# Performance work log

Measured on AMD Instinct MI355X. Metric: run time of the kernel, lower is better.

## Reference

```python
import jax, jax.numpy as jnp
import numpy as np
from jax import lax

B, L, C_IN, H = 2048, 128, 150, 230  # batch, seq_len, 3*word_size, hidden_size

MASK_TABLE = jnp.array([[0., 0., 0.],
                        [1., 0., 0.],
                        [0., 1., 0.],
                        [0., 0., 1.]], dtype=jnp.float32)  # frozen mask embedding


def setup_inputs() -> dict:
    key = jax.random.key(0)
    k1, k2, k3 = jax.random.split(key, 3)
    Xea = jax.random.normal(k1, (B, L, C_IN), dtype=jnp.float32)
    X_mask = jax.random.randint(k2, (B, L), 0, 4)
    # xavier_uniform for Conv1d weight [out, in, kw]
    fan_in, fan_out = C_IN * 3, H * 3
    limit = float(np.sqrt(6.0 / (fan_in + fan_out)))
    W = jax.random.uniform(k3, (H, C_IN, 3), dtype=jnp.float32, minval=-limit, maxval=limit)
    b = jnp.zeros((H,), dtype=jnp.float32)
    return {"Xea": Xea, "X_mask": X_mask, "W": W, "b": b}


def reference(Xea, X_mask, W, b):
    # Xea: [B, L, C_in] -> conv over sequence dim, kernel=3, padding=1
    x = jnp.transpose(Xea, (0, 2, 1))  # [B, C_in, L]
    y = lax.conv_general_dilated(
        x, W, window_strides=(1,), padding=[(1, 1)],
        dimension_numbers=('NCH', 'OIH', 'NCH'))  # [B, H, L]
    y = y + b[None, :, None]
    X = jnp.transpose(y, (0, 2, 1))  # [B, L, H]
    m = MASK_TABLE[X_mask]  # [B, L, 3] one-hot piece indicators (0 row = pad)
    # piecewise max pool: broadcast multiply then max over seq
    pooled = jnp.max(m[:, :, None, :] * X[:, :, :, None], axis=1)  # [B, H, 3]
    return jnp.tanh(pooled.reshape(pooled.shape[0], -1))  # [B, 3*H]
```

## Files before the change

kernel.cpp:

```cpp
#include <hip/hip_runtime.h>
#include <hip/hip_bf16.h>
#include <math.h>


#define B_SZ   2048
#define L_SEQ  128
#define C_INCH 150
#define H_OUT  230
#define RS     152
#define NROW   129
#define NS8    2451

typedef __attribute__((ext_vector_type(8))) short short8;
typedef __attribute__((ext_vector_type(4))) float float4v;

static __device__ __forceinline__ unsigned short f2bf(float f) {
    union { float f; unsigned u; } x{f};
    unsigned r = (x.u + 0x7FFFu + ((x.u >> 16) & 1u)) >> 16;
    return (unsigned short)r;
}

static __device__ __forceinline__ unsigned cvt2(float2 f) {
    __hip_bfloat162 h = __float22bfloat162_rn(f);
    union { __hip_bfloat162 h; unsigned u; } c{h};
    return c.u;
}

static __device__ __forceinline__ float tanh_fast_pos(float v) {
    float e = __expf(2.0f * v);
    return 1.0f - 2.0f / (e + 1.0f);
}

__global__ void pack_w_kernel(const float* __restrict__ W,
                              unsigned short* __restrict__ Wpk) {
    int t = blockIdx.x * 256 + threadIdx.x;
    int kk   = t >> 10;
    int rem  = t & 1023;
    int ht   = rem >> 6;
    int lane = rem & 63;
    int q    = lane >> 4;
    int c15  = lane & 15;
    int k    = kk / 5;
    int kc   = kk - k * 5;
    int h    = ht * 16 + c15;
    int cb   = kc * 32 + q * 8;
    unsigned short v[8];
    #pragma unroll
    for (int e = 0; e < 8; ++e) {
        int c = cb + e;
        float f = (h < H_OUT && c < C_INCH) ? W[h * 450 + c * 3 + k] : 0.0f;
        v[e] = f2bf(f);
    }
    *(short8*)(Wpk + (size_t)t * 8) = *(short8*)v;
}

__global__ void __launch_bounds__(512, 4)
pcnn_mfma(const float* __restrict__ Xea, const int* __restrict__ Xmask,
          const unsigned short* __restrict__ Wpk,
          const float* __restrict__ bias, float* __restrict__ out) {
    __shared__ __align__(16) unsigned short sX[NROW * RS];
    __shared__ __align__(16) float sSel[L_SEQ * 3];

    const int b    = blockIdx.x;
    const int tid  = threadIdx.x;
    const int wv   = tid >> 6;
    const int lane = tid & 63;
    const int q    = lane >> 4;
    const int c15  = lane & 15;
    const int mh   = wv & 1;
    const int nh   = wv >> 1;

    const unsigned short* wp = Wpk + ((size_t)(nh * 4) * 64 + lane) * 8;

    short8 bb[2][4];
    #pragma unroll
    for (int nj = 0; nj < 4; ++nj)
        bb[0][nj] = *(const short8*)(wp + nj * 512);

    const float* xb = Xea + (size_t)b * (L_SEQ * C_INCH);
    float2 pl[5][4];
    #pragma unroll
    for (int it = 0; it < 5; ++it) {
        const int t   = it * 512 + tid;
        const int tc  = (t < NS8) ? t : (NS8 - 1);
        const int row = tc / 19;
        const int j   = tc - row * 19;
        const int rm1 = (row > 0) ? (row - 1) : 0;
        const float* s = xb + rm1 * C_INCH + j * 8;
        pl[it][0] = *(const float2*)(s);
        pl[it][1] = *(const float2*)(s + 2);
        pl[it][2] = *(const float2*)(s + 4);
        pl[it][3] = *(const float2*)(s + ((j < 18) ? 6 : 4));
    }

    if (tid < L_SEQ) {
        int mv = Xmask[(size_t)b * L_SEQ + tid];
        sSel[tid * 3 + 0] = (mv == 1) ? 0.0f : -1e30f;
        sSel[tid * 3 + 1] = (mv == 2) ? 0.0f : -1e30f;
        sSel[tid * 3 + 2] = (mv == 3) ? 0.0f : -1e30f;
    }

    #pragma unroll
    for (int it = 0; it < 5; ++it) {
        const int t   = it * 512 + tid;
        const int tc  = (t < NS8) ? t : (NS8 - 1);
        const int row = tc / 19;
        const int j   = tc - row * 19;
        uint4 u;
        u.x = cvt2(pl[it][0]);
        u.y = cvt2(pl[it][1]);
        u.z = cvt2(pl[it][2]);
        u.w = cvt2(pl[it][3]);
        const bool z = (row == 0);
        u.x = z ? 0u : u.x;
        u.y = z ? 0u : u.y;
        u.z = z ? 0u : u.z;
        u.w = (z || j == 18) ? 0u : u.w;
        if (t < NS8) *(uint4*)(sX + (size_t)t * 8) = u;
    }

    __syncthreads();

    float4v acc[4][4];
    #pragma unroll
    for (int mi = 0; mi < 4; ++mi)
        #pragma unroll
        for (int nj = 0; nj < 4; ++nj)
            acc[mi][nj] = (float4v){0.f, 0.f, 0.f, 0.f};

    const unsigned short* a0p = sX + (mh * 64 + c15) * RS + q * 8;
    const unsigned short* a3p2 = (mh == 1 && c15 == 15) ? (a0p - 129 * RS) : a0p;

    #pragma unroll
    for (int kk = 0; kk < 15; ++kk) {
        const int cur = kk & 1;
        if (kk < 14) {
            #pragma unroll
            for (int nj = 0; nj < 4; ++nj)
                bb[cur ^ 1][nj] =
                    *(const short8*)(wp + (size_t)(kk + 1) * 8192 + nj * 512);
        }
        const int k  = kk / 5;
        const int kc = kk - k * 5;
        short8 a[4];
        #pragma unroll
        for (int mi = 0; mi < 4; ++mi) {
            const unsigned short* base = (mi == 3 && k == 2) ? a3p2 : a0p;
            a[mi] = *(const short8*)(base + (mi * 16 + k) * RS + kc * 32);
        }
        __builtin_amdgcn_s_setprio(1);
        #pragma unroll
        for (int mi = 0; mi < 4; ++mi)
            #pragma unroll
            for (int nj = 0; nj < 4; ++nj)
                acc[mi][nj] = __builtin_amdgcn_mfma_f32_16x16x32_bf16(
                    a[mi], bb[cur][nj], acc[mi][nj], 0, 0, 0);
        __builtin_amdgcn_s_setprio(0);
        __builtin_amdgcn_sched_barrier(0);
    }

    float pz[4][3];
    #pragma unroll
    for (int nj = 0; nj < 4; ++nj)
        #pragma unroll
        for (int p = 0; p < 3; ++p) pz[nj][p] = -1e30f;

    #pragma unroll
    for (int mi = 0; mi < 4; ++mi) {
        const int l0 = mh * 64 + mi * 16 + q * 4;
        const float4v* sp = (const float4v*)(sSel + l0 * 3);
        const float4v s0 = sp[0], s1 = sp[1], s2 = sp[2];
        const float sl[12] = {s0.x, s0.y, s0.z, s0.w, s1.x, s1.y,
                              s1.z, s1.w, s2.x, s2.y, s2.z, s2.w};
        #pragma unroll
        for (int nj = 0; nj < 4; ++nj)
            #pragma unroll
            for (int r = 0; r < 4; ++r) {
                const float y = acc[mi][nj][r];
                pz[nj][0] = fmaxf(pz[nj][0], y + sl[r * 3 + 0]);
                pz[nj][1] = fmaxf(pz[nj][1], y + sl[r * 3 + 1]);
                pz[nj][2] = fmaxf(pz[nj][2], y + sl[r * 3 + 2]);
            }
    }

    __syncthreads();
    float* sP = (float*)sX;

    #pragma unroll
    for (int nj = 0; nj < 4; ++nj) {
        float p0 = pz[nj][0], p1 = pz[nj][1], p2 = pz[nj][2];
        p0 = fmaxf(p0, __shfl_xor(p0, 16, 64));
        p1 = fmaxf(p1, __shfl_xor(p1, 16, 64));
        p2 = fmaxf(p2, __shfl_xor(p2, 16, 64));
        p0 = fmaxf(p0, __shfl_xor(p0, 32, 64));
        p1 = fmaxf(p1, __shfl_xor(p1, 32, 64));
        p2 = fmaxf(p2, __shfl_xor(p2, 32, 64));
        if (q == 0) {
            const int hl = nh * 64 + nj * 16 + c15;
            float* d = sP + (mh * 256 + hl) * 3;
            d[0] = p0; d[1] = p1; d[2] = p2;
        }
    }
    __syncthreads();

    for (int t = tid; t < 768; t += 512) {
        const int h = t / 3;
        const int p = t - h * 3;
        if (h < H_OUT) {
            float v = fmaxf(sP[h * 3 + p], sP[(256 + h) * 3 + p]);
            v = fmaxf(0.0f, v + bias[h]);
            out[(size_t)b * (3 * H_OUT) + h * 3 + p] = tanh_fast_pos(v);
        }
    }
}

extern "C" void kernel_launch(void* const* d_in, const int* in_sizes, int n_in,
                              void* d_out, int out_size, void* d_ws, size_t ws_size,
                              hipStream_t stream) {
    const float* Xea   = (const float*)d_in[0];
    const int*   Xmask = (const int*)d_in[1];
    const float* W     = (const float*)d_in[2];
    const float* bias  = (const float*)d_in[3];
    float* out = (float*)d_out;
    unsigned short* Wpk = (unsigned short*)d_ws;

    pack_w_kernel<<<60, 256, 0, stream>>>(W, Wpk);
    pcnn_mfma<<<B_SZ, 512, 0, stream>>>(Xea, Xmask, Wpk, bias, out);
}
```

Before: 256.3 us.

## Process four batches per block, pairing MFMAs and prefetching next pair during compute

Each block now handles four batch rows instead of one. It computes two rows at once so every weight fragment loaded from global memory is reused across two A tiles. While the first pair is being computed, the block loads, converts and stages the second pair's inputs and masks into LDS. This targets weight reload traffic and exposed global-load latency, at the cost of four times the LDS per block, twice the accumulator registers, fewer blocks (512 on the GPU) and a launch-bounds occupancy target lowered from 4 to 2.

```diff
diff --git a/kernel.cpp b/kernel.cpp
--- a/kernel.cpp
+++ b/kernel.cpp
@@ -10,6 +10,8 @@
 #define RS     152
 #define NROW   129
 #define NS8    2451
+#define TILE   (NROW * RS)
+#define IB     4
 
 typedef __attribute__((ext_vector_type(8))) short short8;
 typedef __attribute__((ext_vector_type(4))) float float4v;
@@ -29,6 +31,95 @@
 static __device__ __forceinline__ float tanh_fast_pos(float v) {
     float e = __expf(2.0f * v);
     return 1.0f - 2.0f / (e + 1.0f);
+}
+
+static __device__ __forceinline__ void stage_load(const float* __restrict__ xb,
+                                                  int tid, int it, float2 pl[4]) {
+    const int t   = it * 512 + tid;
+    const int tc  = (t < NS8) ? t : (NS8 - 1);
+    const int row = tc / 19;
+    const int j   = tc - row * 19;
+    const int rm1 = (row > 0) ? (row - 1) : 0;
+    const float* s = xb + rm1 * C_INCH + j * 8;
+    pl[0] = *(const float2*)(s);
+    pl[1] = *(const float2*)(s + 2);
+    pl[2] = *(const float2*)(s + 4);
+    pl[3] = *(const float2*)(s + ((j < 18) ? 6 : 4));
+}
+
+static __device__ __forceinline__ void stage_write(unsigned short* __restrict__ dst,
+                                                   int tid, int it, const float2 pl[4]) {
+    const int t   = it * 512 + tid;
+    const int tc  = (t < NS8) ? t : (NS8 - 1);
+    const int row = tc / 19;
+    const int j   = tc - row * 19;
+    uint4 u;
+    u.x = cvt2(pl[0]); u.y = cvt2(pl[1]); u.z = cvt2(pl[2]); u.w = cvt2(pl[3]);
+    const bool z = (row == 0);
+    u.x = z ? 0u : u.x;
+    u.y = z ? 0u : u.y;
+    u.z = z ? 0u : u.z;
+    u.w = (z || j == 18) ? 0u : u.w;
+    if (t < NS8) *(uint4*)(dst + (size_t)t * 8) = u;
+}
+
+static __device__ __forceinline__ void epi_partial(const float4v acc[4][4],
+                                                   const float* __restrict__ sel,
+                                                   float* __restrict__ sP,
+                                                   int mh, int nh, int q, int c15) {
+    float pz[4][3];
+    #pragma unroll
+    for (int nj = 0; nj < 4; ++nj)
+        #pragma unroll
+        for (int p = 0; p < 3; ++p) pz[nj][p] = -1e30f;
+
+    #pragma unroll
+    for (int mi = 0; mi < 4; ++mi) {
+        const int l0 = mh * 64 + mi * 16 + q * 4;
+        const float4v* sp = (const float4v*)(sel + l0 * 3);
+        const float4v s0 = sp[0], s1 = sp[1], s2 = sp[2];
+        const float sl[12] = {s0.x, s0.y, s0.z, s0.w, s1.x, s1.y,
+                              s1.z, s1.w, s2.x, s2.y, s2.z, s2.w};
+        #pragma unroll
+        for (int nj = 0; nj < 4; ++nj)
+            #pragma unroll
+            for (int r = 0; r < 4; ++r) {
+                const float y = acc[mi][nj][r];
+                pz[nj][0] = fmaxf(pz[nj][0], y + sl[r * 3 + 0]);
+                pz[nj][1] = fmaxf(pz[nj][1], y + sl[r * 3 + 1]);
+                pz[nj][2] = fmaxf(pz[nj][2], y + sl[r * 3 + 2]);
+            }
+    }
+    #pragma unroll
+    for (int nj = 0; nj < 4; ++nj) {
+        float p0 = pz[nj][0], p1 = pz[nj][1], p2 = pz[nj][2];
+        p0 = fmaxf(p0, __shfl_xor(p0, 16, 64));
+        p1 = fmaxf(p1, __shfl_xor(p1, 16, 64));
+        p2 = fmaxf(p2, __shfl_xor(p2, 16, 64));
+        p0 = fmaxf(p0, __shfl_xor(p0, 32, 64));
+        p1 = fmaxf(p1, __shfl_xor(p1, 32, 64));
+        p2 = fmaxf(p2, __shfl_xor(p2, 32, 64));
+        if (q == 0) {
+            const int hl = nh * 64 + nj * 16 + c15;
+            float* d = sP + (mh * 256 + hl) * 3;
+            d[0] = p0; d[1] = p1; d[2] = p2;
+        }
+    }
+}
+
+static __device__ __forceinline__ void epi_store(float* __restrict__ outb,
+                                                 const float* __restrict__ sP,
+                                                 const float* __restrict__ bias,
+                                                 int tid) {
+    for (int t = tid; t < 768; t += 512) {
+        const int h = t / 3;
+        const int p = t - h * 3;
+        if (h < H_OUT) {
+            float v = fmaxf(sP[h * 3 + p], sP[(256 + h) * 3 + p]);
+            v = fmaxf(0.0f, v + bias[h]);
+            outb[h * 3 + p] = tanh_fast_pos(v);
+        }
+    }
 }
 
 __global__ void pack_w_kernel(const float* __restrict__ W,
@@ -54,14 +145,13 @@
     *(short8*)(Wpk + (size_t)t * 8) = *(short8*)v;
 }
 
-__global__ void __launch_bounds__(512, 4)
+__global__ void __launch_bounds__(512, 2)
 pcnn_mfma(const float* __restrict__ Xea, const int* __restrict__ Xmask,
           const unsigned short* __restrict__ Wpk,
           const float* __restrict__ bias, float* __restrict__ out) {
-    __shared__ __align__(16) unsigned short sX[NROW * RS];
-    __shared__ __align__(16) float sSel[L_SEQ * 3];
-
-    const int b    = blockIdx.x;
+    __shared__ __align__(16) unsigned short sX[4][TILE];
+    __shared__ __align__(16) float sSel[4][L_SEQ * 3];
+
     const int tid  = threadIdx.x;
     const int wv   = tid >> 6;
     const int lane = tid & 63;
@@ -69,6 +159,7 @@
     const int c15  = lane & 15;
     const int mh   = wv & 1;
     const int nh   = wv >> 1;
+    const int b0   = blockIdx.x * IB;
 
     const unsigned short* wp = Wpk + ((size_t)(nh * 4) * 64 + lane) * 8;
 
@@ -77,140 +168,121 @@
     for (int nj = 0; nj < 4; ++nj)
         bb[0][nj] = *(const short8*)(wp + nj * 512);
 
-    const float* xb = Xea + (size_t)b * (L_SEQ * C_INCH);
-    float2 pl[5][4];
-    #pragma unroll
-    for (int it = 0; it < 5; ++it) {
-        const int t   = it * 512 + tid;
-        const int tc  = (t < NS8) ? t : (NS8 - 1);
-        const int row = tc / 19;
-        const int j   = tc - row * 19;
-        const int rm1 = (row > 0) ? (row - 1) : 0;
-        const float* s = xb + rm1 * C_INCH + j * 8;
-        pl[it][0] = *(const float2*)(s);
-        pl[it][1] = *(const float2*)(s + 2);
-        pl[it][2] = *(const float2*)(s + 4);
-        pl[it][3] = *(const float2*)(s + ((j < 18) ? 6 : 4));
-    }
-
-    if (tid < L_SEQ) {
-        int mv = Xmask[(size_t)b * L_SEQ + tid];
-        sSel[tid * 3 + 0] = (mv == 1) ? 0.0f : -1e30f;
-        sSel[tid * 3 + 1] = (mv == 2) ? 0.0f : -1e30f;
-        sSel[tid * 3 + 2] = (mv == 3) ? 0.0f : -1e30f;
-    }
-
-    #pragma unroll
-    for (int it = 0; it < 5; ++it) {
-        const int t   = it * 512 + tid;
-        const int tc  = (t < NS8) ? t : (NS8 - 1);
-        const int row = tc / 19;
-        const int j   = tc - row * 19;
-        uint4 u;
-        u.x = cvt2(pl[it][0]);
-        u.y = cvt2(pl[it][1]);
-        u.z = cvt2(pl[it][2]);
-        u.w = cvt2(pl[it][3]);
-        const bool z = (row == 0);
-        u.x = z ? 0u : u.x;
-        u.y = z ? 0u : u.y;
-        u.z = z ? 0u : u.z;
-        u.w = (z || j == 18) ? 0u : u.w;
-        if (t < NS8) *(uint4*)(sX + (size_t)t * 8) = u;
-    }
-
+    {
+        const float* xb0 = Xea + (size_t)b0 * (L_SEQ * C_INCH);
+        float2 pA[5][4];
+        #pragma unroll
+        for (int it = 0; it < 5; ++it) stage_load(xb0, tid, it, pA[it]);
+        if (tid < L_SEQ) {
+            const int m0 = Xmask[(size_t)b0 * L_SEQ + tid];
+            const int m1 = Xmask[(size_t)(b0 + 1) * L_SEQ + tid];
+            sSel[0][tid * 3 + 0] = (m0 == 1) ? 0.0f : -1e30f;
+            sSel[0][tid * 3 + 1] = (m0 == 2) ? 0.0f : -1e30f;
+            sSel[0][tid * 3 + 2] = (m0 == 3) ? 0.0f : -1e30f;
+            sSel[1][tid * 3 + 0] = (m1 == 1) ? 0.0f : -1e30f;
+            sSel[1][tid * 3 + 1] = (m1 == 2) ? 0.0f : -1e30f;
+            sSel[1][tid * 3 + 2] = (m1 == 3) ? 0.0f : -1e30f;
+        }
+        #pragma unroll
+        for (int it = 0; it < 5; ++it) stage_write(sX[0], tid, it, pA[it]);
+        const float* xb1 = xb0 + L_SEQ * C_INCH;
+        float2 pB[5][4];
+        #pragma unroll
+        for (int it = 0; it < 5; ++it) stage_load(xb1, tid, it, pB[it]);
+        #pragma unroll
+        for (int it = 0; it < 5; ++it) stage_write(sX[1], tid, it, pB[it]);
+    }
     __syncthreads();
 
-    float4v acc[4][4];
-    #pragma unroll
-    for (int mi = 0; mi < 4; ++mi)
-        #pragma unroll
-        for (int nj = 0; nj < 4; ++nj)
-            acc[mi][nj] = (float4v){0.f, 0.f, 0.f, 0.f};
-
-    const unsigned short* a0p = sX + (mh * 64 + c15) * RS + q * 8;
-    const unsigned short* a3p2 = (mh == 1 && c15 == 15) ? (a0p - 129 * RS) : a0p;
-
-    #pragma unroll
-    for (int kk = 0; kk < 15; ++kk) {
-        const int cur = kk & 1;
-        if (kk < 14) {
-            #pragma unroll
-            for (int nj = 0; nj < 4; ++nj)
-                bb[cur ^ 1][nj] =
-                    *(const short8*)(wp + (size_t)(kk + 1) * 8192 + nj * 512);
+    float2 stg[3][4];
+    int mvA = 0, mvB = 0;
+
+    #pragma unroll
+    for (int pr = 0; pr < 2; ++pr) {
+        const int bA = b0 + 2 * pr;
+
+        float4v accA[4][4], accB[4][4];
+        #pragma unroll
+        for (int mi = 0; mi < 4; ++mi)
+            #pragma unroll
+            for (int nj = 0; nj < 4; ++nj) {
+                accA[mi][nj] = (float4v){0.f, 0.f, 0.f, 0.f};
+                accB[mi][nj] = (float4v){0.f, 0.f, 0.f, 0.f};
+            }
+
+        const unsigned short* a0pA = sX[2 * pr]     + (mh * 64 + c15) * RS + q * 8;
+        const unsigned short* a0pB = sX[2 * pr + 1] + (mh * 64 + c15) * RS + q * 8;
+        const unsigned short* a3pA = (mh == 1 && c15 == 15) ? (a0pA - 129 * RS) : a0pA;
+        const unsigned short* a3pB = (mh == 1 && c15 == 15) ? (a0pB - 129 * RS) : a0pB;
+
+        #pragma unroll
+        for (int kk = 0; kk < 15; ++kk) {
+            const int g   = pr * 15 + kk;
+            const int cur = g & 1;
+            if (g < 29) {
+                const int kn = (g + 1) % 15;
+                #pragma unroll
+                for (int nj = 0; nj < 4; ++nj)
+                    bb[cur ^ 1][nj] =
+                        *(const short8*)(wp + (size_t)kn * 8192 + nj * 512);
+            }
+            const int k  = kk / 5;
+            const int kc = kk - k * 5;
+            short8 aA[4], aB[4];
+            #pragma unroll
+            for (int mi = 0; mi < 4; ++mi) {
+                const unsigned short* pA_ = (mi == 3 && k == 2) ? a3pA : a0pA;
+                const unsigned short* pB_ = (mi == 3 && k == 2) ? a3pB : a0pB;
+                aA[mi] = *(const short8*)(pA_ + (mi * 16 + k) * RS + kc * 32);
+                aB[mi] = *(const short8*)(pB_ + (mi * 16 + k) * RS + kc * 32);
+            }
+            if (pr == 0 && kk >= 1 && kk <= 10) {
+                const int s = kk - 1;
+                const float* xs =
+                    Xea + (size_t)(b0 + 2 + (s >= 5 ? 1 : 0)) * (L_SEQ * C_INCH);
+                stage_load(xs, tid, s % 5, stg[s % 3]);
+            }
+            if (pr == 0 && kk == 13 && tid < L_SEQ) {
+                mvA = Xmask[(size_t)(b0 + 2) * L_SEQ + tid];
+                mvB = Xmask[(size_t)(b0 + 3) * L_SEQ + tid];
+            }
+            __builtin_amdgcn_s_setprio(1);
+            #pragma unroll
+            for (int mi = 0; mi < 4; ++mi)
+                #pragma unroll
+                for (int nj = 0; nj < 4; ++nj)
+                    accA[mi][nj] = __builtin_amdgcn_mfma_f32_16x16x32_bf16(
+                        aA[mi], bb[cur][nj], accA[mi][nj], 0, 0, 0);
+            #pragma unroll
+            for (int mi = 0; mi < 4; ++mi)
+                #pragma unroll
+                for (int nj = 0; nj < 4; ++nj)
+                    accB[mi][nj] = __builtin_amdgcn_mfma_f32_16x16x32_bf16(
+                        aB[mi], bb[cur][nj], accB[mi][nj], 0, 0, 0);
+            __builtin_amdgcn_s_setprio(0);
+            if (pr == 0 && kk >= 3 && kk <= 12) {
+                const int s = kk - 3;
+                stage_write(sX[2 + (s >= 5 ? 1 : 0)], tid, s % 5, stg[s % 3]);
+            }
+            if (pr == 0 && kk == 14 && tid < L_SEQ) {
+                sSel[2][tid * 3 + 0] = (mvA == 1) ? 0.0f : -1e30f;
+                sSel[2][tid * 3 + 1] = (mvA == 2) ? 0.0f : -1e30f;
+                sSel[2][tid * 3 + 2] = (mvA == 3) ? 0.0f : -1e30f;
+                sSel[3][tid * 3 + 0] = (mvB == 1) ? 0.0f : -1e30f;
+                sSel[3][tid * 3 + 1] = (mvB == 2) ? 0.0f : -1e30f;
+                sSel[3][tid * 3 + 2] = (mvB == 3) ? 0.0f : -1e30f;
+            }
+            __builtin_amdgcn_sched_barrier(0);
         }
-        const int k  = kk / 5;
-        const int kc = kk - k * 5;
-        short8 a[4];
-        #pragma unroll
-        for (int mi = 0; mi < 4; ++mi) {
-            const unsigned short* base = (mi == 3 && k == 2) ? a3p2 : a0p;
-            a[mi] = *(const short8*)(base + (mi * 16 + k) * RS + kc * 32);
-        }
-        __builtin_amdgcn_s_setprio(1);
-        #pragma unroll
-        for (int mi = 0; mi < 4; ++mi)
-            #pragma unroll
-            for (int nj = 0; nj < 4; ++nj)
-                acc[mi][nj] = __builtin_amdgcn_mfma_f32_16x16x32_bf16(
-                    a[mi], bb[cur][nj], acc[mi][nj], 0, 0, 0);
-        __builtin_amdgcn_s_setprio(0);
-        __builtin_amdgcn_sched_barrier(0);
-    }
-
-    float pz[4][3];
-    #pragma unroll
-    for (int nj = 0; nj < 4; ++nj)
-        #pragma unroll
-        for (int p = 0; p < 3; ++p) pz[nj][p] = -1e30f;
-
-    #pragma unroll
-    for (int mi = 0; mi < 4; ++mi) {
-        const int l0 = mh * 64 + mi * 16 + q * 4;
-        const float4v* sp = (const float4v*)(sSel + l0 * 3);
-        const float4v s0 = sp[0], s1 = sp[1], s2 = sp[2];
-        const float sl[12] = {s0.x, s0.y, s0.z, s0.w, s1.x, s1.y,
-                              s1.z, s1.w, s2.x, s2.y, s2.z, s2.w};
-        #pragma unroll
-        for (int nj = 0; nj < 4; ++nj)
-            #pragma unroll
-            for (int r = 0; r < 4; ++r) {
-                const float y = acc[mi][nj][r];
-                pz[nj][0] = fmaxf(pz[nj][0], y + sl[r * 3 + 0]);
-                pz[nj][1] = fmaxf(pz[nj][1], y + sl[r * 3 + 1]);
-                pz[nj][2] = fmaxf(pz[nj][2], y + sl[r * 3 + 2]);
-            }
-    }
-
-    __syncthreads();
-    float* sP = (float*)sX;
-
-    #pragma unroll
-    for (int nj = 0; nj < 4; ++nj) {
-        float p0 = pz[nj][0], p1 = pz[nj][1], p2 = pz[nj][2];
-        p0 = fmaxf(p0, __shfl_xor(p0, 16, 64));
-        p1 = fmaxf(p1, __shfl_xor(p1, 16, 64));
-        p2 = fmaxf(p2, __shfl_xor(p2, 16, 64));
-        p0 = fmaxf(p0, __shfl_xor(p0, 32, 64));
-        p1 = fmaxf(p1, __shfl_xor(p1, 32, 64));
-        p2 = fmaxf(p2, __shfl_xor(p2, 32, 64));
-        if (q == 0) {
-            const int hl = nh * 64 + nj * 16 + c15;
-            float* d = sP + (mh * 256 + hl) * 3;
-            d[0] = p0; d[1] = p1; d[2] = p2;
-        }
-    }
-    __syncthreads();
-
-    for (int t = tid; t < 768; t += 512) {
-        const int h = t / 3;
-        const int p = t - h * 3;
-        if (h < H_OUT) {
-            float v = fmaxf(sP[h * 3 + p], sP[(256 + h) * 3 + p]);
-            v = fmaxf(0.0f, v + bias[h]);
-            out[(size_t)b * (3 * H_OUT) + h * 3 + p] = tanh_fast_pos(v);
-        }
+
+        __syncthreads();
+        epi_partial(accA, sSel[2 * pr],     (float*)sX[2 * pr],     mh, nh, q, c15);
+        epi_partial(accB, sSel[2 * pr + 1], (float*)sX[2 * pr + 1], mh, nh, q, c15);
+        __syncthreads();
+        epi_store(out + (size_t)bA * (3 * H_OUT),
+                  (const float*)sX[2 * pr], bias, tid);
+        epi_store(out + (size_t)(bA + 1) * (3 * H_OUT),
+                  (const float*)sX[2 * pr + 1], bias, tid);
     }
 }
 
@@ -225,5 +297,5 @@
     unsigned short* Wpk = (unsigned short*)d_ws;
 
     pack_w_kernel<<<60, 256, 0, stream>>>(W, Wpk);
-    pcnn_mfma<<<B_SZ, 512, 0, stream>>>(Xea, Xmask, Wpk, bias, out);
-}
+    pcnn_mfma<<<B_SZ / IB, 512, 0, stream>>>(Xea, Xmask, Wpk, bias, out);
+}
```

After: 291.2 us. 1.14x slower.

## Split output channels across two blocks per batch with XCD-aware mapping

Applied to the files above, without the earlier changes.

Each batch is now handled by two workgroups, each computing half of the hidden channels (128 each), which halves per-wave accumulators and B-fragment registers. Launch bounds are raised to 6 waves-per-EU, and block IDs are remapped so both halves of a batch land on the same XCD, letting the second block's load of the same X rows hit in L2. The input staging is split into two smaller load/write phases to reduce live registers. The trade-off is that the X tile is staged into shared memory twice per batch, doubling LDS staging and conversion work.

```diff
diff --git a/kernel.cpp b/kernel.cpp
--- a/kernel.cpp
+++ b/kernel.cpp
@@ -29,6 +29,36 @@
 static __device__ __forceinline__ float tanh_fast_pos(float v) {
     float e = __expf(2.0f * v);
     return 1.0f - 2.0f / (e + 1.0f);
+}
+
+static __device__ __forceinline__ void stage_load(const float* __restrict__ xb,
+                                                  int tid, int it, float2 pl[4]) {
+    const int t   = it * 512 + tid;
+    const int tc  = (t < NS8) ? t : (NS8 - 1);
+    const int row = tc / 19;
+    const int j   = tc - row * 19;
+    const int rm1 = (row > 0) ? (row - 1) : 0;
+    const float* s = xb + rm1 * C_INCH + j * 8;
+    pl[0] = *(const float2*)(s);
+    pl[1] = *(const float2*)(s + 2);
+    pl[2] = *(const float2*)(s + 4);
+    pl[3] = *(const float2*)(s + ((j < 18) ? 6 : 4));
+}
+
+static __device__ __forceinline__ void stage_write(unsigned short* __restrict__ dst,
+                                                   int tid, int it, const float2 pl[4]) {
+    const int t   = it * 512 + tid;
+    const int tc  = (t < NS8) ? t : (NS8 - 1);
+    const int row = tc / 19;
+    const int j   = tc - row * 19;
+    uint4 u;
+    u.x = cvt2(pl[0]); u.y = cvt2(pl[1]); u.z = cvt2(pl[2]); u.w = cvt2(pl[3]);
+    const bool z = (row == 0);
+    u.x = z ? 0u : u.x;
+    u.y = z ? 0u : u.y;
+    u.z = z ? 0u : u.z;
+    u.w = (z || j == 18) ? 0u : u.w;
+    if (t < NS8) *(uint4*)(dst + (size_t)t * 8) = u;
 }
 
 __global__ void pack_w_kernel(const float* __restrict__ W,
@@ -54,78 +84,61 @@
     *(short8*)(Wpk + (size_t)t * 8) = *(short8*)v;
 }
 
-__global__ void __launch_bounds__(512, 4)
+__global__ void __launch_bounds__(512, 6)
 pcnn_mfma(const float* __restrict__ Xea, const int* __restrict__ Xmask,
           const unsigned short* __restrict__ Wpk,
           const float* __restrict__ bias, float* __restrict__ out) {
     __shared__ __align__(16) unsigned short sX[NROW * RS];
     __shared__ __align__(16) float sSel[L_SEQ * 3];
 
-    const int b    = blockIdx.x;
     const int tid  = threadIdx.x;
     const int wv   = tid >> 6;
     const int lane = tid & 63;
     const int q    = lane >> 4;
     const int c15  = lane & 15;
     const int mh   = wv & 1;
-    const int nh   = wv >> 1;
-
-    const unsigned short* wp = Wpk + ((size_t)(nh * 4) * 64 + lane) * 8;
-
-    short8 bb[2][4];
-    #pragma unroll
-    for (int nj = 0; nj < 4; ++nj)
+    const int nq   = wv >> 1;
+
+    const int g    = blockIdx.x;
+    const int xcd  = g & 7;
+    const int rest = g >> 3;
+    const int b    = xcd * 256 + (rest >> 1);
+    const int nbh  = rest & 1;
+
+    const unsigned short* wp =
+        Wpk + ((size_t)((nbh * 8 + nq * 2) * 64) + lane) * 8;
+
+    short8 bb[2][2];
+    #pragma unroll
+    for (int nj = 0; nj < 2; ++nj)
         bb[0][nj] = *(const short8*)(wp + nj * 512);
 
     const float* xb = Xea + (size_t)b * (L_SEQ * C_INCH);
-    float2 pl[5][4];
-    #pragma unroll
-    for (int it = 0; it < 5; ++it) {
-        const int t   = it * 512 + tid;
-        const int tc  = (t < NS8) ? t : (NS8 - 1);
-        const int row = tc / 19;
-        const int j   = tc - row * 19;
-        const int rm1 = (row > 0) ? (row - 1) : 0;
-        const float* s = xb + rm1 * C_INCH + j * 8;
-        pl[it][0] = *(const float2*)(s);
-        pl[it][1] = *(const float2*)(s + 2);
-        pl[it][2] = *(const float2*)(s + 4);
-        pl[it][3] = *(const float2*)(s + ((j < 18) ? 6 : 4));
-    }
-
-    if (tid < L_SEQ) {
-        int mv = Xmask[(size_t)b * L_SEQ + tid];
-        sSel[tid * 3 + 0] = (mv == 1) ? 0.0f : -1e30f;
-        sSel[tid * 3 + 1] = (mv == 2) ? 0.0f : -1e30f;
-        sSel[tid * 3 + 2] = (mv == 3) ? 0.0f : -1e30f;
-    }
-
-    #pragma unroll
-    for (int it = 0; it < 5; ++it) {
-        const int t   = it * 512 + tid;
-        const int tc  = (t < NS8) ? t : (NS8 - 1);
-        const int row = tc / 19;
-        const int j   = tc - row * 19;
-        uint4 u;
-        u.x = cvt2(pl[it][0]);
-        u.y = cvt2(pl[it][1]);
-        u.z = cvt2(pl[it][2]);
-        u.w = cvt2(pl[it][3]);
-        const bool z = (row == 0);
-        u.x = z ? 0u : u.x;
-        u.y = z ? 0u : u.y;
-        u.z = z ? 0u : u.z;
-        u.w = (z || j == 18) ? 0u : u.w;
-        if (t < NS8) *(uint4*)(sX + (size_t)t * 8) = u;
+    {
+        float2 pl[3][4];
+        #pragma unroll
+        for (int it = 0; it < 3; ++it) stage_load(xb, tid, it, pl[it]);
+        if (tid < L_SEQ) {
+            int mv = Xmask[(size_t)b * L_SEQ + tid];
+            sSel[tid * 3 + 0] = (mv == 1) ? 0.0f : -1e30f;
+            sSel[tid * 3 + 1] = (mv == 2) ? 0.0f : -1e30f;
+            sSel[tid * 3 + 2] = (mv == 3) ? 0.0f : -1e30f;
+        }
+        #pragma unroll
+        for (int it = 0; it < 3; ++it) stage_write(sX, tid, it, pl[it]);
+        #pragma unroll
+        for (int it = 0; it < 2; ++it) stage_load(xb, tid, 3 + it, pl[it]);
+        #pragma unroll
+        for (int it = 0; it < 2; ++it) stage_write(sX, tid, 3 + it, pl[it]);
     }
 
     __syncthreads();
 
-    float4v acc[4][4];
+    float4v acc[4][2];
     #pragma unroll
     for (int mi = 0; mi < 4; ++mi)
         #pragma unroll
-        for (int nj = 0; nj < 4; ++nj)
+        for (int nj = 0; nj < 2; ++nj)
             acc[mi][nj] = (float4v){0.f, 0.f, 0.f, 0.f};
 
     const unsigned short* a0p = sX + (mh * 64 + c15) * RS + q * 8;
@@ -136,7 +149,7 @@
         const int cur = kk & 1;
         if (kk < 14) {
             #pragma unroll
-            for (int nj = 0; nj < 4; ++nj)
+            for (int nj = 0; nj < 2; ++nj)
                 bb[cur ^ 1][nj] =
                     *(const short8*)(wp + (size_t)(kk + 1) * 8192 + nj * 512);
         }
@@ -152,16 +165,16 @@
         #pragma unroll
         for (int mi = 0; mi < 4; ++mi)
             #pragma unroll
-            for (int nj = 0; nj < 4; ++nj)
+            for (int nj = 0; nj < 2; ++nj)
                 acc[mi][nj] = __builtin_amdgcn_mfma_f32_16x16x32_bf16(
                     a[mi], bb[cur][nj], acc[mi][nj], 0, 0, 0);
         __builtin_amdgcn_s_setprio(0);
         __builtin_amdgcn_sched_barrier(0);
     }
 
-    float pz[4][3];
-    #pragma unroll
-    for (int nj = 0; nj < 4; ++nj)
+    float pz[2][3];
+    #pragma unroll
+    for (int nj = 0; nj < 2; ++nj)
         #pragma unroll
         for (int p = 0; p < 3; ++p) pz[nj][p] = -1e30f;
 
@@ -173,7 +186,7 @@
         const float sl[12] = {s0.x, s0.y, s0.z, s0.w, s1.x, s1.y,
                               s1.z, s1.w, s2.x, s2.y, s2.z, s2.w};
         #pragma unroll
-        for (int nj = 0; nj < 4; ++nj)
+        for (int nj = 0; nj < 2; ++nj)
             #pragma unroll
             for (int r = 0; r < 4; ++r) {
                 const float y = acc[mi][nj][r];
@@ -187,7 +200,7 @@
     float* sP = (float*)sX;
 
     #pragma unroll
-    for (int nj = 0; nj < 4; ++nj) {
+    for (int nj = 0; nj < 2; ++nj) {
         float p0 = pz[nj][0], p1 = pz[nj][1], p2 = pz[nj][2];
         p0 = fmaxf(p0, __shfl_xor(p0, 16, 64));
         p1 = fmaxf(p1, __shfl_xor(p1, 16, 64));
@@ -196,18 +209,19 @@
         p1 = fmaxf(p1, __shfl_xor(p1, 32, 64));
         p2 = fmaxf(p2, __shfl_xor(p2, 32, 64));
         if (q == 0) {
-            const int hl = nh * 64 + nj * 16 + c15;
-            float* d = sP + (mh * 256 + hl) * 3;
+            const int hl = nq * 32 + nj * 16 + c15;
+            float* d = sP + (mh * 128 + hl) * 3;
             d[0] = p0; d[1] = p1; d[2] = p2;
         }
     }
     __syncthreads();
 
-    for (int t = tid; t < 768; t += 512) {
-        const int h = t / 3;
-        const int p = t - h * 3;
+    for (int t = tid; t < 384; t += 512) {
+        const int hl = t / 3;
+        const int p  = t - hl * 3;
+        const int h  = nbh * 128 + hl;
         if (h < H_OUT) {
-            float v = fmaxf(sP[h * 3 + p], sP[(256 + h) * 3 + p]);
+            float v = fmaxf(sP[hl * 3 + p], sP[(128 + hl) * 3 + p]);
             v = fmaxf(0.0f, v + bias[h]);
             out[(size_t)b * (3 * H_OUT) + h * 3 + p] = tanh_fast_pos(v);
         }
@@ -225,5 +239,5 @@
     unsigned short* Wpk = (unsigned short*)d_ws;
 
     pack_w_kernel<<<60, 256, 0, stream>>>(W, Wpk);
-    pcnn_mfma<<<B_SZ, 512, 0, stream>>>(Xea, Xmask, Wpk, bias, out);
-}
+    pcnn_mfma<<<B_SZ * 2, 512, 0, stream>>>(Xea, Xmask, Wpk, bias, out);
+}
```

Measured after the change: 264.9 us. 1.03x slower.
